# Kernel optimization log

Hardware: AMD Instinct MI355X
Metric: run time of the kernel (lower is better)

## Reference

```python
import jax, jax.numpy as jnp
import numpy as np

N_FFT = 2048
HOP = 512
N_FREQ = N_FFT // 2 + 1  # 1025


def _dft_conv_weights():
    # periodic ('fftbins=True') Hann window, matching librosa get_window('hann', N, fftbins=True)
    n = np.arange(N_FFT)
    win = 0.5 - 0.5 * np.cos(2.0 * np.pi * n / N_FFT)
    k = np.arange(N_FREQ)
    ang = 2.0 * np.pi * np.outer(k, n) / N_FFT  # (F, n_fft)
    # W[n, k] = exp(-2*pi*i*n*k/N); real part = cos, imag part = -sin; windowed per-tap
    w_real = (np.cos(ang) * win[None, :]).astype(np.float32)
    w_imag = (-np.sin(ang) * win[None, :]).astype(np.float32)
    return w_real, w_imag


def setup_inputs() -> dict:
    key = jax.random.key(0)
    x = jax.random.normal(key, (16, 320000), dtype=jnp.float32)
    w_real, w_imag = _dft_conv_weights()
    return {
        "input": x,
        "conv_real_w": jnp.asarray(w_real),
        "conv_imag_w": jnp.asarray(w_imag),
    }


def reference(input, conv_real_w, conv_imag_w):
    # center=True: reflect-pad n_fft//2 on both sides
    pad = N_FFT // 2
    x = jnp.pad(input, ((0, 0), (pad, pad)), mode="reflect")  # (B, L + n_fft)
    L = x.shape[1]
    T = (L - N_FFT) // HOP + 1  # time_steps
    # frame extraction == Conv1d with kernel n_fft, stride hop
    idx = jnp.arange(T)[:, None] * HOP + jnp.arange(N_FFT)[None, :]  # (T, n_fft)
    frames = x[:, idx]  # (B, T, n_fft)
    real = jnp.einsum("btn,fn->bft", frames, conv_real_w)  # (B, F, T)
    imag = jnp.einsum("btn,fn->bft", frames, conv_imag_w)  # (B, F, T)
    return real, imag
```

## Files before the change

kernel.cpp:

```cpp
#include <hip/hip_runtime.h>

#define B_BATCH 16
#define XLEN    320000
#define NFFT    2048
#define HOP     512
#define PADW    1024
#define NFREQ   1025
#define T_OUT   626
#define M_ROWS  2050
#define NCOLS   (B_BATCH * T_OUT)
#define MT2     17
#define NT2     40
#define NBLK    (MT2 * NT2)
#define KT2     32

#define XPAD_LEN    322048
#define XPAD_STRIDE 330240
#define APACK_BYTES ((size_t)MT2 * 64 * 8192)
#define XPAD_BYTES  ((size_t)(B_BATCH + 1) * XPAD_STRIDE * 2)
#define WS_NEEDED   (APACK_BYTES + XPAD_BYTES)

typedef __bf16 bf16x8 __attribute__((ext_vector_type(8)));
typedef __bf16 bf16x4 __attribute__((ext_vector_type(4)));
typedef float  f32x4  __attribute__((ext_vector_type(4)));

__device__ __forceinline__ void gload_lds16(const void* g, void* l) {
    __builtin_amdgcn_global_load_lds(
        (const __attribute__((address_space(1))) unsigned int*)g,
        (__attribute__((address_space(3))) unsigned int*)l,
        16, 0, 0);
}

__global__ __launch_bounds__(256) void prep_w(
    const float* __restrict__ wre, const float* __restrict__ wim,
    __bf16* __restrict__ apack)
{
    const int gid   = blockIdx.x * 256 + threadIdx.x;
    const int scell = gid & 3;
    const int row   = (gid >> 2) & 127;
    const int ph    = (gid >> 9) & 63;
    const int mt    = gid >> 15;

    const int grow = mt * 128 + row;
    const int k    = ph * 32 + (((scell ^ (row >> 1)) & 3) << 3);

    bf16x8 v = bf16x8{};
    if (grow < M_ROWS) {
        const float* src = (grow < NFREQ)
            ? (wre + (size_t)grow * NFFT + k)
            : (wim + (size_t)(grow - NFREQ) * NFFT + k);
        const float4 a = *reinterpret_cast<const float4*>(src);
        const float4 b = *reinterpret_cast<const float4*>(src + 4);
        v[0] = (__bf16)a.x; v[1] = (__bf16)a.y; v[2] = (__bf16)a.z; v[3] = (__bf16)a.w;
        v[4] = (__bf16)b.x; v[5] = (__bf16)b.y; v[6] = (__bf16)b.z; v[7] = (__bf16)b.w;
    }
    *reinterpret_cast<bf16x8*>(apack + (size_t)gid * 8) = v;
}

__global__ __launch_bounds__(256) void prep_x(
    const float* __restrict__ x, __bf16* __restrict__ xpad)
{
    const int gid = blockIdx.x * 256 + threadIdx.x;
    if (gid >= (B_BATCH + 1) * (XPAD_STRIDE / 8)) return;
    const int b  = gid / (XPAD_STRIDE / 8);
    const int i0 = (gid - b * (XPAD_STRIDE / 8)) * 8;

    bf16x8 v = bf16x8{};
    if (b < B_BATCH) {
        const float* xb = x + (size_t)b * XLEN;
        const int pos0 = i0 - PADW;
        if (pos0 >= 0 && pos0 + 8 <= XLEN) {
            const float4 a = *reinterpret_cast<const float4*>(xb + pos0);
            const float4 c = *reinterpret_cast<const float4*>(xb + pos0 + 4);
            v[0] = (__bf16)a.x; v[1] = (__bf16)a.y; v[2] = (__bf16)a.z; v[3] = (__bf16)a.w;
            v[4] = (__bf16)c.x; v[5] = (__bf16)c.y; v[6] = (__bf16)c.z; v[7] = (__bf16)c.w;
        } else {
            #pragma unroll
            for (int e = 0; e < 8; ++e) {
                const int i = i0 + e;
                if (i >= XPAD_LEN) { v[e] = (__bf16)0.f; continue; }
                int p = i - PADW;
                p = (p < 0) ? -p : p;
                p = (p >= XLEN) ? (2 * XLEN - 2 - p) : p;
                v[e] = (__bf16)xb[p];
            }
        }
    }
    *reinterpret_cast<bf16x8*>(xpad + (size_t)b * XPAD_STRIDE + i0) = v;
}


#define MFMA16 __builtin_amdgcn_mfma_f32_16x16x32_bf16

#define VM3 asm volatile("s_waitcnt vmcnt(3)" ::: "memory");
#define VM0 asm volatile("s_waitcnt vmcnt(0)" ::: "memory");

#define STG(PH_, SLOT_) {                                                         \
    gload_lds16(ablk + ((size_t)(PH_) << 13),                                     \
                lds + ((SLOT_) << 13) + (wid << 10));                             \
    {                                                                             \
        const int ko_ = (PH_) << 6;                                               \
        unsigned char* d_ = lds + 24576 + ((SLOT_) << 14) + (wid << 10);          \
        gload_lds16(gb0 + ko_, d_);                                               \
        gload_lds16(gb1 + ko_, d_ + 8192);                                        \
    }                                                                             \
}

#define PH(SLOT_, STG_, VMW_) {                                                   \
    bf16x8 a0, a1, a2, a3, b0, b1, b2, b3;                                        \
    {                                                                             \
        const unsigned ab_ = ((unsigned)(SLOT_) << 13) + offA_base;               \
        const unsigned bb_ = 24576u + ((unsigned)(SLOT_) << 14) + offB_base;      \
        a0 = *(const bf16x8*)(lds + ab_);                                         \
        a1 = *(const bf16x8*)(lds + ab_ + 1024);                                  \
        a2 = *(const bf16x8*)(lds + ab_ + 2048);                                  \
        a3 = *(const bf16x8*)(lds + ab_ + 3072);                                  \
        b0 = *(const bf16x8*)(lds + bb_);                                         \
        b1 = *(const bf16x8*)(lds + bb_ + 1024);                                  \
        b2 = *(const bf16x8*)(lds + bb_ + 2048);                                  \
        b3 = *(const bf16x8*)(lds + bb_ + 3072);                                  \
    }                                                                             \
    STG_                                                                          \
    VMW_                                                                          \
    __builtin_amdgcn_s_barrier();                                                 \
    asm volatile("s_waitcnt lgkmcnt(0)" ::: "memory");                            \
    __builtin_amdgcn_sched_barrier(0);                                            \
    __builtin_amdgcn_s_setprio(1);                                                \
    acc[0][0] = MFMA16(a0, b0, acc[0][0], 0, 0, 0);                               \
    acc[0][1] = MFMA16(a0, b1, acc[0][1], 0, 0, 0);                               \
    acc[0][2] = MFMA16(a0, b2, acc[0][2], 0, 0, 0);                               \
    acc[0][3] = MFMA16(a0, b3, acc[0][3], 0, 0, 0);                               \
    acc[1][0] = MFMA16(a1, b0, acc[1][0], 0, 0, 0);                               \
    acc[1][1] = MFMA16(a1, b1, acc[1][1], 0, 0, 0);                               \
    acc[1][2] = MFMA16(a1, b2, acc[1][2], 0, 0, 0);                               \
    acc[1][3] = MFMA16(a1, b3, acc[1][3], 0, 0, 0);                               \
    acc[2][0] = MFMA16(a2, b0, acc[2][0], 0, 0, 0);                               \
    acc[2][1] = MFMA16(a2, b1, acc[2][1], 0, 0, 0);                               \
    acc[2][2] = MFMA16(a2, b2, acc[2][2], 0, 0, 0);                               \
    acc[2][3] = MFMA16(a2, b3, acc[2][3], 0, 0, 0);                               \
    acc[3][0] = MFMA16(a3, b0, acc[3][0], 0, 0, 0);                               \
    acc[3][1] = MFMA16(a3, b1, acc[3][1], 0, 0, 0);                               \
    acc[3][2] = MFMA16(a3, b2, acc[3][2], 0, 0, 0);                               \
    acc[3][3] = MFMA16(a3, b3, acc[3][3], 0, 0, 0);                               \
    __builtin_amdgcn_s_setprio(0);                                                \
}

__global__ __launch_bounds__(512, 4) void stft_gemm7(
    const __bf16* __restrict__ apack,
    const __bf16* __restrict__ xpad,
    float* __restrict__ out)
{
    __shared__ __align__(16) unsigned char lds[73728];

    const int tid  = threadIdx.x;
    const int lane = tid & 63;
    const int wid  = tid >> 6;
    const int wm   = wid >> 2;
    const int wn   = wid & 3;
    const int fr   = lane & 15;
    const int kq   = lane >> 4;

    const int orig = (blockIdx.x & 7) * 85 + (blockIdx.x >> 3);
    const int nt = orig / MT2;
    const int mt = orig % MT2;

    const char* ablk = (const char*)apack + (size_t)mt * (64 * 8192) + (size_t)tid * 16;

    const char* xpb = (const char*)xpad;
    const char* gb0;
    const char* gb1;
    {
        const int r0 = tid >> 2;
        const int sc = (tid & 3) ^ ((r0 >> 1) & 3);
        int col = nt * 256 + r0;
        unsigned b = (unsigned)col / 626u;
        int tc = col - (int)b * 626;
        gb0 = xpb + ((size_t)b * XPAD_STRIDE + (size_t)tc * 512) * 2 + sc * 16;
        col += 128;
        b = (unsigned)col / 626u;
        tc = col - (int)b * 626;
        gb1 = xpb + ((size_t)b * XPAD_STRIDE + (size_t)tc * 512) * 2 + sc * 16;
    }

    const unsigned swz = (unsigned)(((kq ^ (fr >> 1)) & 3) << 4);
    const unsigned offA_base = (unsigned)((wm * 64 + fr) * 64) + swz;
    const unsigned offB_base = (unsigned)((wn * 64 + fr) * 64) + swz;

    f32x4 acc[4][4];
    #pragma unroll
    for (int m = 0; m < 4; ++m)
        #pragma unroll
        for (int n = 0; n < 4; ++n)
            acc[m][n] = f32x4{0.f, 0.f, 0.f, 0.f};

    STG(0, 0)
    STG(1, 1)
    VM3
    __builtin_amdgcn_s_barrier();
    __builtin_amdgcn_sched_barrier(0);

    #pragma unroll 1
    for (int i = 0; i < 10; ++i) {
        const int t = 6 * i;
        PH(0, STG(t + 2, 2), VM3)
        PH(1, STG(t + 3, 0), VM3)
        PH(2, STG(t + 4, 1), VM3)
        PH(0, STG(t + 5, 2), VM3)
        PH(1, STG(t + 6, 0), VM3)
        PH(2, STG(t + 7, 1), VM3)
    }
    PH(0, STG(62, 2), VM3)
    PH(1, STG(63, 0), VM3)
    PH(2, , VM0)
    PH(0, , )

    const size_t imag_base = (size_t)B_BATCH * NFREQ * T_OUT;
    #pragma unroll
    for (int n = 0; n < 4; ++n) {
        const int col = nt * 256 + wn * 64 + n * 16 + fr;
        if (col < NCOLS) {
            const unsigned b = (unsigned)col / 626u;
            const int tc = col - (int)b * 626;
            const size_t colbase = (size_t)b * NFREQ * T_OUT + (size_t)tc;
            #pragma unroll
            for (int m = 0; m < 4; ++m) {
                #pragma unroll
                for (int j = 0; j < 4; ++j) {
                    const int grow = mt * 128 + wm * 64 + m * 16 + kq * 4 + j;
                    if (grow < M_ROWS) {
                        const size_t off = (grow < NFREQ)
                            ? colbase + (size_t)grow * T_OUT
                            : imag_base + colbase + (size_t)(grow - NFREQ) * T_OUT;
                        out[off] = acc[m][n][j];
                    }
                }
            }
        }
    }
}

__device__ __forceinline__ unsigned lds_off_fb(int row, int kbyte) {
    return (unsigned)(row * 128 + (kbyte ^ ((row & 7) << 4)));
}

__global__ __launch_bounds__(256) void stft_gemm_fb(
    const float* __restrict__ x,
    const float* __restrict__ wre,
    const float* __restrict__ wim,
    float* __restrict__ out)
{
    __shared__ __align__(16) unsigned char ldsA[128 * 128];
    __shared__ __align__(16) unsigned char ldsB[128 * 128];

    const int tid  = threadIdx.x;
    const int lane = tid & 63;
    const int wid  = tid >> 6;
    const int wmf  = wid >> 1;
    const int wnf  = wid & 1;

    const int bid = blockIdx.x;
    const int b   = bid / (17 * 5);
    const int rem = bid % (17 * 5);
    const int mt  = rem / 5;
    const int nt  = rem % 5;

    const int row0 = mt * 128;
    const int col0 = nt * 128;
    const float* xb = x + (size_t)b * XLEN;

    const int c4 = (tid & 15) * 4;
    const int r0 = tid >> 4;

    f32x4 acc[4][4];
    #pragma unroll
    for (int m = 0; m < 4; ++m)
        #pragma unroll
        for (int n = 0; n < 4; ++n)
            acc[m][n] = f32x4{0.f, 0.f, 0.f, 0.f};

    const int fr = lane & 15;
    const int kq = lane >> 4;

    for (int k0 = 0; k0 < NFFT; k0 += 64) {
        bf16x4 sa[8], sb[8];
        #pragma unroll
        for (int rr = 0; rr < 8; ++rr) {
            const int row  = rr * 16 + r0;
            const int grow = row0 + row;
            float4 v = make_float4(0.f, 0.f, 0.f, 0.f);
            if (grow < M_ROWS) {
                const float* wsrc = (grow < NFREQ)
                    ? (wre + (size_t)grow * NFFT)
                    : (wim + (size_t)(grow - NFREQ) * NFFT);
                v = *reinterpret_cast<const float4*>(wsrc + k0 + c4);
            }
            sa[rr].x = (__bf16)v.x; sa[rr].y = (__bf16)v.y;
            sa[rr].z = (__bf16)v.z; sa[rr].w = (__bf16)v.w;
        }
        #pragma unroll
        for (int rr = 0; rr < 8; ++rr) {
            const int trow = rr * 16 + r0;
            const int t    = col0 + trow;
            float4 v = make_float4(0.f, 0.f, 0.f, 0.f);
            if (t < T_OUT) {
                const int pos = t * HOP + k0 + c4 - PADW;
                if (pos >= 0 && pos <= XLEN - 4) {
                    v = *reinterpret_cast<const float4*>(xb + pos);
                } else {
                    float tmp[4];
                    #pragma unroll
                    for (int e = 0; e < 4; ++e) {
                        int p = pos + e;
                        p = (p < 0) ? -p : p;
                        p = (p >= XLEN) ? (2 * XLEN - 2 - p) : p;
                        tmp[e] = xb[p];
                    }
                    v = make_float4(tmp[0], tmp[1], tmp[2], tmp[3]);
                }
            }
            sb[rr].x = (__bf16)v.x; sb[rr].y = (__bf16)v.y;
            sb[rr].z = (__bf16)v.z; sb[rr].w = (__bf16)v.w;
        }
        __syncthreads();
        #pragma unroll
        for (int rr = 0; rr < 8; ++rr) {
            const int row = rr * 16 + r0;
            *reinterpret_cast<bf16x4*>(ldsA + lds_off_fb(row, c4 * 2)) = sa[rr];
            *reinterpret_cast<bf16x4*>(ldsB + lds_off_fb(row, c4 * 2)) = sb[rr];
        }
        __syncthreads();
        #pragma unroll
        for (int kk = 0; kk < 2; ++kk) {
            const int kbyte = kk * 64 + kq * 16;
            bf16x8 af[4], bfv[4];
            #pragma unroll
            for (int m = 0; m < 4; ++m)
                af[m] = *reinterpret_cast<const bf16x8*>(
                    ldsA + lds_off_fb(wmf * 64 + m * 16 + fr, kbyte));
            #pragma unroll
            for (int n = 0; n < 4; ++n)
                bfv[n] = *reinterpret_cast<const bf16x8*>(
                    ldsB + lds_off_fb(wnf * 64 + n * 16 + fr, kbyte));
            #pragma unroll
            for (int m = 0; m < 4; ++m)
                #pragma unroll
                for (int n = 0; n < 4; ++n)
                    acc[m][n] = MFMA16(af[m], bfv[n], acc[m][n], 0, 0, 0);
        }
    }

    const size_t imag_base = (size_t)B_BATCH * NFREQ * T_OUT;
    #pragma unroll
    for (int m = 0; m < 4; ++m) {
        #pragma unroll
        for (int n = 0; n < 4; ++n) {
            #pragma unroll
            for (int j = 0; j < 4; ++j) {
                const int grow = row0 + wmf * 64 + m * 16 + kq * 4 + j;
                const int gcol = col0 + wnf * 64 + n * 16 + fr;
                if (grow < M_ROWS && gcol < T_OUT) {
                    size_t off;
                    if (grow < NFREQ)
                        off = ((size_t)b * NFREQ + grow) * T_OUT + gcol;
                    else
                        off = imag_base + ((size_t)b * NFREQ + (grow - NFREQ)) * T_OUT + gcol;
                    out[off] = acc[m][n][j];
                }
            }
        }
    }
}

extern "C" void kernel_launch(void* const* d_in, const int* in_sizes, int n_in,
                              void* d_out, int out_size, void* d_ws, size_t ws_size,
                              hipStream_t stream) {
    const float* x   = (const float*)d_in[0];
    const float* wre = (const float*)d_in[1];
    const float* wim = (const float*)d_in[2];
    float* out = (float*)d_out;

    if (ws_size < WS_NEEDED) {
        stft_gemm_fb<<<dim3(B_BATCH * 17 * 5), 256, 0, stream>>>(x, wre, wim, out);
        return;
    }

    __bf16* apack = (__bf16*)d_ws;
    __bf16* xpad  = (__bf16*)((char*)d_ws + APACK_BYTES);

    prep_w<<<dim3(557056 / 256), 256, 0, stream>>>(wre, wim, apack);
    prep_x<<<dim3(((B_BATCH + 1) * (XPAD_STRIDE / 8) + 255) / 256), 256, 0, stream>>>(x, xpad);
    stft_gemm7<<<dim3(NBLK), 512, 0, stream>>>(apack, xpad, out);
}
```

Before: 113.7 us.

## Load A operand directly from global into registers, deepen B LDS pipeline

The weight (A) tiles no longer go through LDS. Each wave now reads its A fragments straight from global memory into double-buffered registers, one phase ahead. The freed LDS holds a fourth B stage, so the B pipeline runs three phases ahead with adjusted vmcnt waits. B fragments are read with inline-asm ds_read_b128, and the MFMA issue order is changed to iterate over A fragments inside each B column. This removes LDS write and read traffic for A, at the cost of redundant global and L2 reads for A across the waves that share a row block, plus higher register pressure.

```diff
diff --git a/kernel.cpp b/kernel.cpp
--- a/kernel.cpp
+++ b/kernel.cpp
@@ -92,65 +92,66 @@
 
 #define MFMA16 __builtin_amdgcn_mfma_f32_16x16x32_bf16
 
-#define VM3 asm volatile("s_waitcnt vmcnt(3)" ::: "memory");
+#define VM8 asm volatile("s_waitcnt vmcnt(8)" ::: "memory");
+#define VM4 asm volatile("s_waitcnt vmcnt(4)" ::: "memory");
 #define VM0 asm volatile("s_waitcnt vmcnt(0)" ::: "memory");
 
-#define STG(PH_, SLOT_) {                                                         \
-    gload_lds16(ablk + ((size_t)(PH_) << 13),                                     \
-                lds + ((SLOT_) << 13) + (wid << 10));                             \
+#define STGB(PH_, SLOT_) {                                                        \
+    unsigned char* d_ = lds + ((SLOT_) << 14) + (wid << 10);                      \
+    gload_lds16(gb0 + ((PH_) << 6), d_);                                          \
+    gload_lds16(gb1 + ((PH_) << 6), d_ + 8192);                                   \
+}
+
+#define ALD(PH_, DST_) {                                                          \
+    const char* ap_ = ag + ((unsigned)(PH_) << 13);                               \
+    DST_[0] = *(const bf16x8*)(ap_);                                              \
+    DST_[1] = *(const bf16x8*)(ap_ + 1024);                                       \
+    DST_[2] = *(const bf16x8*)(ap_ + 2048);                                       \
+    DST_[3] = *(const bf16x8*)(ap_ + 3072);                                       \
+}
+
+#define PH(SLOT_, CUR_, ALOAD_, STG_, VMW_) {                                     \
+    bf16x8 b0_, b1_, b2_, b3_;                                                    \
     {                                                                             \
-        const int ko_ = (PH_) << 6;                                               \
-        unsigned char* d_ = lds + 24576 + ((SLOT_) << 14) + (wid << 10);          \
-        gload_lds16(gb0 + ko_, d_);                                               \
-        gload_lds16(gb1 + ko_, d_ + 8192);                                        \
+        const unsigned bb_ = ((unsigned)(SLOT_) << 14) + offB_base;               \
+        asm volatile("ds_read_b128 %0, %1"             : "=v"(b0_) : "v"(bb_));   \
+        asm volatile("ds_read_b128 %0, %1 offset:1024" : "=v"(b1_) : "v"(bb_));   \
+        asm volatile("ds_read_b128 %0, %1 offset:2048" : "=v"(b2_) : "v"(bb_));   \
+        asm volatile("ds_read_b128 %0, %1 offset:3072" : "=v"(b3_) : "v"(bb_));   \
     }                                                                             \
-}
-
-#define PH(SLOT_, STG_, VMW_) {                                                   \
-    bf16x8 a0, a1, a2, a3, b0, b1, b2, b3;                                        \
-    {                                                                             \
-        const unsigned ab_ = ((unsigned)(SLOT_) << 13) + offA_base;               \
-        const unsigned bb_ = 24576u + ((unsigned)(SLOT_) << 14) + offB_base;      \
-        a0 = *(const bf16x8*)(lds + ab_);                                         \
-        a1 = *(const bf16x8*)(lds + ab_ + 1024);                                  \
-        a2 = *(const bf16x8*)(lds + ab_ + 2048);                                  \
-        a3 = *(const bf16x8*)(lds + ab_ + 3072);                                  \
-        b0 = *(const bf16x8*)(lds + bb_);                                         \
-        b1 = *(const bf16x8*)(lds + bb_ + 1024);                                  \
-        b2 = *(const bf16x8*)(lds + bb_ + 2048);                                  \
-        b3 = *(const bf16x8*)(lds + bb_ + 3072);                                  \
-    }                                                                             \
+    ALOAD_                                                                        \
     STG_                                                                          \
+    __builtin_amdgcn_sched_barrier(0);                                            \
     VMW_                                                                          \
     __builtin_amdgcn_s_barrier();                                                 \
     asm volatile("s_waitcnt lgkmcnt(0)" ::: "memory");                            \
     __builtin_amdgcn_sched_barrier(0);                                            \
     __builtin_amdgcn_s_setprio(1);                                                \
-    acc[0][0] = MFMA16(a0, b0, acc[0][0], 0, 0, 0);                               \
-    acc[0][1] = MFMA16(a0, b1, acc[0][1], 0, 0, 0);                               \
-    acc[0][2] = MFMA16(a0, b2, acc[0][2], 0, 0, 0);                               \
-    acc[0][3] = MFMA16(a0, b3, acc[0][3], 0, 0, 0);                               \
-    acc[1][0] = MFMA16(a1, b0, acc[1][0], 0, 0, 0);                               \
-    acc[1][1] = MFMA16(a1, b1, acc[1][1], 0, 0, 0);                               \
-    acc[1][2] = MFMA16(a1, b2, acc[1][2], 0, 0, 0);                               \
-    acc[1][3] = MFMA16(a1, b3, acc[1][3], 0, 0, 0);                               \
-    acc[2][0] = MFMA16(a2, b0, acc[2][0], 0, 0, 0);                               \
-    acc[2][1] = MFMA16(a2, b1, acc[2][1], 0, 0, 0);                               \
-    acc[2][2] = MFMA16(a2, b2, acc[2][2], 0, 0, 0);                               \
-    acc[2][3] = MFMA16(a2, b3, acc[2][3], 0, 0, 0);                               \
-    acc[3][0] = MFMA16(a3, b0, acc[3][0], 0, 0, 0);                               \
-    acc[3][1] = MFMA16(a3, b1, acc[3][1], 0, 0, 0);                               \
-    acc[3][2] = MFMA16(a3, b2, acc[3][2], 0, 0, 0);                               \
-    acc[3][3] = MFMA16(a3, b3, acc[3][3], 0, 0, 0);                               \
+    acc[0][0] = MFMA16(CUR_[0], b0_, acc[0][0], 0, 0, 0);                         \
+    acc[1][0] = MFMA16(CUR_[1], b0_, acc[1][0], 0, 0, 0);                         \
+    acc[2][0] = MFMA16(CUR_[2], b0_, acc[2][0], 0, 0, 0);                         \
+    acc[3][0] = MFMA16(CUR_[3], b0_, acc[3][0], 0, 0, 0);                         \
+    acc[0][1] = MFMA16(CUR_[0], b1_, acc[0][1], 0, 0, 0);                         \
+    acc[1][1] = MFMA16(CUR_[1], b1_, acc[1][1], 0, 0, 0);                         \
+    acc[2][1] = MFMA16(CUR_[2], b1_, acc[2][1], 0, 0, 0);                         \
+    acc[3][1] = MFMA16(CUR_[3], b1_, acc[3][1], 0, 0, 0);                         \
+    acc[0][2] = MFMA16(CUR_[0], b2_, acc[0][2], 0, 0, 0);                         \
+    acc[1][2] = MFMA16(CUR_[1], b2_, acc[1][2], 0, 0, 0);                         \
+    acc[2][2] = MFMA16(CUR_[2], b2_, acc[2][2], 0, 0, 0);                         \
+    acc[3][2] = MFMA16(CUR_[3], b2_, acc[3][2], 0, 0, 0);                         \
+    acc[0][3] = MFMA16(CUR_[0], b3_, acc[0][3], 0, 0, 0);                         \
+    acc[1][3] = MFMA16(CUR_[1], b3_, acc[1][3], 0, 0, 0);                         \
+    acc[2][3] = MFMA16(CUR_[2], b3_, acc[2][3], 0, 0, 0);                         \
+    acc[3][3] = MFMA16(CUR_[3], b3_, acc[3][3], 0, 0, 0);                         \
     __builtin_amdgcn_s_setprio(0);                                                \
 }
 
-__global__ __launch_bounds__(512, 4) void stft_gemm7(
+__global__ __launch_bounds__(512, 4) void stft_gemm9(
     const __bf16* __restrict__ apack,
     const __bf16* __restrict__ xpad,
     float* __restrict__ out)
 {
-    __shared__ __align__(16) unsigned char lds[73728];
+    __shared__ __align__(16) unsigned char lds[65536];
 
     const int tid  = threadIdx.x;
     const int lane = tid & 63;
@@ -164,7 +165,10 @@
     const int nt = orig / MT2;
     const int mt = orig % MT2;
 
-    const char* ablk = (const char*)apack + (size_t)mt * (64 * 8192) + (size_t)tid * 16;
+    const unsigned swz = (unsigned)(((kq ^ (fr >> 1)) & 3) << 4);
+
+    const char* ag = (const char*)apack + (size_t)mt * 524288
+                     + (unsigned)((wm * 64 + fr) * 64) + swz;
 
     const char* xpb = (const char*)xpad;
     const char* gb0;
@@ -182,8 +186,6 @@
         gb1 = xpb + ((size_t)b * XPAD_STRIDE + (size_t)tc * 512) * 2 + sc * 16;
     }
 
-    const unsigned swz = (unsigned)(((kq ^ (fr >> 1)) & 3) << 4);
-    const unsigned offA_base = (unsigned)((wm * 64 + fr) * 64) + swz;
     const unsigned offB_base = (unsigned)((wn * 64 + fr) * 64) + swz;
 
     f32x4 acc[4][4];
@@ -193,26 +195,29 @@
         for (int n = 0; n < 4; ++n)
             acc[m][n] = f32x4{0.f, 0.f, 0.f, 0.f};
 
-    STG(0, 0)
-    STG(1, 1)
-    VM3
+    bf16x8 aP[4], aQ[4];
+
+    ALD(0, aP)
+    STGB(0, 0)
+    STGB(1, 1)
+    STGB(2, 2)
+    __builtin_amdgcn_sched_barrier(0);
+    VM4
     __builtin_amdgcn_s_barrier();
     __builtin_amdgcn_sched_barrier(0);
 
     #pragma unroll 1
-    for (int i = 0; i < 10; ++i) {
-        const int t = 6 * i;
-        PH(0, STG(t + 2, 2), VM3)
-        PH(1, STG(t + 3, 0), VM3)
-        PH(2, STG(t + 4, 1), VM3)
-        PH(0, STG(t + 5, 2), VM3)
-        PH(1, STG(t + 6, 0), VM3)
-        PH(2, STG(t + 7, 1), VM3)
-    }
-    PH(0, STG(62, 2), VM3)
-    PH(1, STG(63, 0), VM3)
-    PH(2, , VM0)
-    PH(0, , )
+    for (int i = 0; i < 15; ++i) {
+        const int t = 4 * i;
+        PH(0, aP, ALD(t + 1, aQ), STGB(t + 3, 3), VM8)
+        PH(1, aQ, ALD(t + 2, aP), STGB(t + 4, 0), VM8)
+        PH(2, aP, ALD(t + 3, aQ), STGB(t + 5, 1), VM8)
+        PH(3, aQ, ALD(t + 4, aP), STGB(t + 6, 2), VM8)
+    }
+    PH(0, aP, ALD(61, aQ), STGB(63, 3), VM8)
+    PH(1, aQ, ALD(62, aP), , VM8)
+    PH(2, aP, ALD(63, aQ), , VM4)
+    PH(3, aQ, , , VM0)
 
     const size_t imag_base = (size_t)B_BATCH * NFREQ * T_OUT;
     #pragma unroll
@@ -389,5 +394,5 @@
 
     prep_w<<<dim3(557056 / 256), 256, 0, stream>>>(wre, wim, apack);
     prep_x<<<dim3(((B_BATCH + 1) * (XPAD_STRIDE / 8) + 255) / 256), 256, 0, stream>>>(x, xpad);
-    stft_gemm7<<<dim3(NBLK), 512, 0, stream>>>(apack, xpad, out);
-}
+    stft_gemm9<<<dim3(NBLK), 512, 0, stream>>>(apack, xpad, out);
+}
```

Measured after the change: 174.3 us. 1.53x slower.
